# Kernel tuning notes

Measured on AMD Instinct MI355X. Metric: run time of the kernel, lower is better.

Reference implementation:

```python
import jax, jax.numpy as jnp
import numpy as np

H = 768       # hidden_size
NH = 12       # num_attention_heads
HD = H // NH  # head_size
FF = 3072     # intermediate_size
EPS = 1e-5


def _layernorm(x, g, b):
    m = jnp.mean(x, axis=-1, keepdims=True)
    v = jnp.var(x, axis=-1, keepdims=True)
    return (x - m) * jax.lax.rsqrt(v + EPS) * g + b


def setup_inputs() -> dict:
    key = jax.random.key(0)
    ks = jax.random.split(key, 12)
    B, Sq, Skv = 8, 1024, 1024
    s = 0.02
    return {
        "freq_hidden_states": jax.random.normal(ks[0], (B, Sq, H), jnp.float32),
        "image_hidden_states": jax.random.normal(ks[1], (B, Skv, H), jnp.float32),
        # attention projections (stored [in, out])
        "Wq": jax.random.normal(ks[2], (H, H), jnp.float32) * s,
        "bq": jnp.zeros((H,), jnp.float32),
        "Wk": jax.random.normal(ks[3], (H, H), jnp.float32) * s,
        "bk": jnp.zeros((H,), jnp.float32),
        "Wv": jax.random.normal(ks[4], (H, H), jnp.float32) * s,
        "bv": jnp.zeros((H,), jnp.float32),
        # layernorms
        "ln_att_g": jnp.ones((H,), jnp.float32),
        "ln_att_b": jnp.zeros((H,), jnp.float32),
        "ln_mlp_g": jnp.ones((H,), jnp.float32),
        "ln_mlp_b": jnp.zeros((H,), jnp.float32),
        # MLP
        "W1": jax.random.normal(ks[5], (H, FF), jnp.float32) * s,
        "b1": jnp.zeros((FF,), jnp.float32),
        "W2": jax.random.normal(ks[6], (FF, H), jnp.float32) * s,
        "b2": jnp.zeros((H,), jnp.float32),
    }


def reference(image_hidden_states, freq_hidden_states, Wq, bq, Wk, bk, Wv, bv,
              ln_att_g, ln_att_b, ln_mlp_g, ln_mlp_b, W1, b1, W2, b2):
    B, Sq, _ = freq_hidden_states.shape
    Skv = image_hidden_states.shape[1]
    # cross-attention: query from freq, key/value from image
    q = (freq_hidden_states @ Wq + bq).reshape(B, Sq, NH, HD)
    k = (image_hidden_states @ Wk + bk).reshape(B, Skv, NH, HD)
    v = (image_hidden_states @ Wv + bv).reshape(B, Skv, NH, HD)
    scores = jnp.einsum("bqhd,bkhd->bhqk", q, k) / jnp.sqrt(jnp.float32(HD))
    probs = jax.nn.softmax(scores, axis=-1)
    ctx = jnp.einsum("bhqk,bkhd->bqhd", probs, v).reshape(B, Sq, H)
    # residual with post-LN on the attention output
    h = freq_hidden_states + _layernorm(ctx, ln_att_g, ln_att_b)
    # MLP + residual with post-LN on the MLP output
    mlp = jax.nn.relu(h @ W1 + b1) @ W2 + b2
    return h + _layernorm(mlp, ln_mlp_g, ln_mlp_b)
```

## Files before the change

kernel.cpp:

```cpp
#include <hip/hip_runtime.h>
#include <hip/hip_bf16.h>

#define H 768
#define NH 12
#define HD 64
#define FF 3072
#define SQ 1024
#define SKV 1024

typedef __hip_bfloat16 bf16;
typedef __attribute__((ext_vector_type(8))) short short8;
typedef __attribute__((ext_vector_type(4))) float f32x4;

__device__ inline void gload16(const void* g, void* l) {
  __builtin_amdgcn_global_load_lds((const __attribute__((address_space(1))) void*)g,
                                   (__attribute__((address_space(3))) void*)l, 16, 0, 0);
}

__device__ inline float bf2f(unsigned short u) {
  unsigned int x = ((unsigned int)u) << 16;
  return __builtin_bit_cast(float, x);
}

__global__ __launch_bounds__(256) void cvt_bf16(const float* __restrict__ src,
                                                bf16* __restrict__ dst) {
  int i = blockIdx.x * 256 + threadIdx.x;
  float4 v = ((const float4*)src)[i];
  union { unsigned short u[4]; uint2 q; } o;
  bf16 t0 = __float2bfloat16(v.x); o.u[0] = *(unsigned short*)&t0;
  bf16 t1 = __float2bfloat16(v.y); o.u[1] = *(unsigned short*)&t1;
  bf16 t2 = __float2bfloat16(v.z); o.u[2] = *(unsigned short*)&t2;
  bf16 t3 = __float2bfloat16(v.w); o.u[3] = *(unsigned short*)&t3;
  ((uint2*)dst)[i] = o.q;
}

__global__ __launch_bounds__(256) void trans_cvt(const float* __restrict__ src,
                                                 bf16* __restrict__ dst, int Kd, int Nd) {
  __shared__ float tile[32][33];
  int n0 = blockIdx.x * 32, k0 = blockIdx.y * 32;
  int tx = threadIdx.x, ty = threadIdx.y;
#pragma unroll
  for (int i = 0; i < 4; ++i)
    tile[ty + i * 8][tx] = src[(size_t)(k0 + ty + i * 8) * Nd + n0 + tx];
  __syncthreads();
#pragma unroll
  for (int i = 0; i < 4; ++i)
    dst[(size_t)(n0 + ty + i * 8) * Kd + k0 + tx] = __float2bfloat16(tile[tx][ty + i * 8]);
}

template <int EPI>
__global__ __launch_bounds__(256) void gemm_bt(
    const bf16* __restrict__ A, const bf16* __restrict__ BT,
    const float* __restrict__ bias0, const float* __restrict__ bias1,
    void* __restrict__ out0, void* __restrict__ out1, int M, int N, int K) {
  __shared__ __align__(16) bf16 lA[128 * 64];
  __shared__ __align__(16) bf16 lB[128 * 64];
  const int t = threadIdx.x;
  const int lane = t & 63, w = t >> 6;
  const int wr = w >> 1, wc = w & 1;
  const int nt = N >> 7;
  const int nwg = gridDim.x;
  int bid = blockIdx.x;
  int logical = ((nwg & 7) == 0) ? ((bid & 7) * (nwg >> 3) + (bid >> 3)) : bid;
  const int m0 = (logical / nt) << 7;
  const int n0 = (logical % nt) << 7;

  const f32x4 fz = {0.f, 0.f, 0.f, 0.f};
  f32x4 acc[4][4];
#pragma unroll
  for (int i = 0; i < 4; ++i)
#pragma unroll
    for (int j = 0; j < 4; ++j) acc[i][j] = fz;

  for (int kt = 0; kt < K; kt += 64) {
#pragma unroll
    for (int i = 0; i < 4; ++i) {
      int idx = i * 256 + t;
      int row = idx >> 3;
      int chunk = (idx & 7) ^ (row & 7);
      gload16(A + (size_t)(m0 + row) * K + kt + chunk * 8, lA + (size_t)(i * 256 + w * 64) * 8);
    }
#pragma unroll
    for (int i = 0; i < 4; ++i) {
      int idx = i * 256 + t;
      int row = idx >> 3;
      int chunk = (idx & 7) ^ (row & 7);
      gload16(BT + (size_t)(n0 + row) * K + kt + chunk * 8, lB + (size_t)(i * 256 + w * 64) * 8);
    }
    __syncthreads();

    short8 af[2][4], bfv[2][4];
#pragma unroll
    for (int s = 0; s < 2; ++s) {
#pragma unroll
      for (int i = 0; i < 4; ++i) {
        int ra = wr * 64 + i * 16 + (lane & 15);
        int ca = (s * 4 + (lane >> 4)) ^ (ra & 7);
        af[s][i] = *(const short8*)&lA[ra * 64 + ca * 8];
        int rb = wc * 64 + i * 16 + (lane & 15);
        int cb = (s * 4 + (lane >> 4)) ^ (rb & 7);
        bfv[s][i] = *(const short8*)&lB[rb * 64 + cb * 8];
      }
    }
#pragma unroll
    for (int s = 0; s < 2; ++s)
#pragma unroll
      for (int i = 0; i < 4; ++i)
#pragma unroll
        for (int j = 0; j < 4; ++j)
          acc[i][j] = __builtin_amdgcn_mfma_f32_16x16x32_bf16(af[s][i], bfv[s][j], acc[i][j], 0, 0, 0);
    __syncthreads();
  }

#pragma unroll
  for (int i = 0; i < 4; ++i) {
    int mbase = m0 + wr * 64 + i * 16 + ((lane >> 4) << 2);
#pragma unroll
    for (int j = 0; j < 4; ++j) {
      int n = n0 + wc * 64 + j * 16 + (lane & 15);
#pragma unroll
      for (int r = 0; r < 4; ++r) {
        int m = mbase + r;
        float v = acc[i][j][r];
        if (EPI == 0) {
          v = (v + bias0[n]) * 0.180336880f;
          int hlin = (m >> 10) * NH + (n >> 6);
          ((bf16*)out0)[((size_t)hlin * SQ + (m & 1023)) * HD + (n & 63)] = __float2bfloat16(v);
        } else if (EPI == 1) {
          int sel = (n >= H);
          int nn = n - (sel ? H : 0);
          v += (sel ? bias1 : bias0)[nn];
          int hlin = (m >> 10) * NH + (nn >> 6);
          if (!sel)
            ((bf16*)out0)[((size_t)hlin * SKV + (m & 1023)) * HD + (nn & 63)] = __float2bfloat16(v);
          else
            ((bf16*)out1)[((size_t)hlin * HD + (nn & 63)) * SKV + (m & 1023)] = __float2bfloat16(v);
        } else if (EPI == 2) {
          v += bias0[n];
          v = fmaxf(v, 0.f);
          ((bf16*)out0)[(size_t)m * N + n] = __float2bfloat16(v);
        } else {
          v += bias0[n];
          ((bf16*)out0)[(size_t)m * N + n] = __float2bfloat16(v);
        }
      }
    }
  }
}

__global__ __launch_bounds__(512, 4) void attn_fwd(
    const bf16* __restrict__ Q,
    const bf16* __restrict__ Kg_,
    const bf16* __restrict__ VT,
    bf16* __restrict__ ctx, int nblk) {
  __shared__ __align__(16) bf16 Ks[2][64 * 64];
  __shared__ __align__(16) bf16 Vs[2][64 * 64];
  __shared__ __align__(16) bf16 PQ[8 * 16 * 72];

  const int t = threadIdx.x, lane = t & 63, w = t >> 6;
  int bid = blockIdx.x;
  int logical = ((nblk & 7) == 0) ? (bid & 7) * (nblk >> 3) + (bid >> 3) : bid;
  const int hl = logical >> 3;
  const int q0 = (logical & 7) << 7;
  const bf16* Qg = Q + ((size_t)hl * SQ + q0) * HD;
  const bf16* Kg = Kg_ + (size_t)hl * SKV * HD;
  const bf16* Vg = VT + (size_t)hl * HD * SKV;

#pragma unroll
  for (int rep = 0; rep < 2; ++rep) {
    int idx = rep * 512 + t;
    int row = idx >> 3;
    int chunk = (idx & 7) ^ (row & 7);
    gload16(Qg + (size_t)row * HD + chunk * 8, PQ + (size_t)(rep * 512 + w * 64) * 8);
  }
  {
    int row = t >> 3, chunk = (t & 7) ^ (row & 7);
    gload16(Kg + (size_t)row * HD + chunk * 8, &Ks[0][(size_t)w * 64 * 8]);
    gload16(Vg + (size_t)row * SKV + chunk * 8, &Vs[0][(size_t)w * 64 * 8]);
  }
  __syncthreads();

  short8 aq[2];
#pragma unroll
  for (int s = 0; s < 2; ++s) {
    int row = w * 16 + (lane & 15);
    int chunk = (s * 4 + (lane >> 4)) ^ (row & 7);
    aq[s] = *(const short8*)&PQ[row * 64 + chunk * 8];
  }
  __syncthreads();

  float l_r[4];
#pragma unroll
  for (int r = 0; r < 4; ++r) l_r[r] = 0.f;
  const f32x4 fz = {0.f, 0.f, 0.f, 0.f};
  f32x4 oacc[4];
#pragma unroll
  for (int j = 0; j < 4; ++j) oacc[j] = fz;

  bf16* Pw = PQ + w * (16 * 72);
  const short s1 = (short)0x3F80;
  const short8 ones = {s1, s1, s1, s1, s1, s1, s1, s1};

#pragma unroll 2
  for (int i = 0; i < 16; ++i) {
    const int buf = i & 1;
    if (i < 15) {
      int kvn = (i + 1) << 6;
      int row = t >> 3, chunk = (t & 7) ^ (row & 7);
      gload16(Kg + (size_t)(kvn + row) * HD + chunk * 8, &Ks[buf ^ 1][(size_t)w * 64 * 8]);
      gload16(Vg + (size_t)row * SKV + kvn + chunk * 8, &Vs[buf ^ 1][(size_t)w * 64 * 8]);
    }

    f32x4 sa[4];
#pragma unroll
    for (int n = 0; n < 4; ++n) sa[n] = fz;
    __builtin_amdgcn_s_setprio(1);
#pragma unroll
    for (int s = 0; s < 2; ++s)
#pragma unroll
      for (int n = 0; n < 4; ++n) {
        int rb = n * 16 + (lane & 15);
        int cb = (s * 4 + (lane >> 4)) ^ (rb & 7);
        short8 bk = *(const short8*)&Ks[buf][rb * 64 + cb * 8];
        sa[n] = __builtin_amdgcn_mfma_f32_16x16x32_bf16(aq[s], bk, sa[n], 0, 0, 0);
      }
    __builtin_amdgcn_s_setprio(0);

#pragma unroll
    for (int n = 0; n < 4; ++n)
#pragma unroll
      for (int r = 0; r < 4; ++r)
        Pw[(((lane >> 4) << 2) + r) * 72 + n * 16 + (lane & 15)] =
            __float2bfloat16(exp2f(sa[n][r]));

    f32x4 ld = fz;
    __builtin_amdgcn_s_setprio(1);
#pragma unroll
    for (int kk = 0; kk < 2; ++kk) {
      short8 pa = *(const short8*)&Pw[(lane & 15) * 72 + kk * 32 + ((lane >> 4) << 3)];
      ld = __builtin_amdgcn_mfma_f32_16x16x32_bf16(pa, ones, ld, 0, 0, 0);
#pragma unroll
      for (int j = 0; j < 4; ++j) {
        int rb = j * 16 + (lane & 15);
        int cb = (kk * 4 + (lane >> 4)) ^ (rb & 7);
        short8 bv = *(const short8*)&Vs[buf][rb * 64 + cb * 8];
        oacc[j] = __builtin_amdgcn_mfma_f32_16x16x32_bf16(pa, bv, oacc[j], 0, 0, 0);
      }
    }
    __builtin_amdgcn_s_setprio(0);
#pragma unroll
    for (int r = 0; r < 4; ++r) l_r[r] += ld[r];

    __syncthreads();
  }

  const int b = hl / NH, hh = hl % NH;
  float rl[4];
#pragma unroll
  for (int r = 0; r < 4; ++r) rl[r] = 1.0f / l_r[r];
#pragma unroll
  for (int j = 0; j < 4; ++j)
#pragma unroll
    for (int r = 0; r < 4; ++r) {
      int q = q0 + w * 16 + ((lane >> 4) << 2) + r;
      int d = j * 16 + (lane & 15);
      ctx[((size_t)b * SQ + q) * H + hh * HD + d] = __float2bfloat16(oacc[j][r] * rl[r]);
    }
}

__global__ __launch_bounds__(256) void ln_res(
    const bf16* __restrict__ x, const float* __restrict__ res,
    const float* __restrict__ g, const float* __restrict__ beta,
    float* __restrict__ o32, bf16* __restrict__ ob, int write_b) {
  const int row = blockIdx.x;
  const int t = threadIdx.x;
  float v[4];
  float s = 0.f, s2 = 0.f;
  if (t < 192) {
    ushort4 xv = ((const ushort4*)(x + (size_t)row * H))[t];
    v[0] = bf2f(xv.x); v[1] = bf2f(xv.y); v[2] = bf2f(xv.z); v[3] = bf2f(xv.w);
#pragma unroll
    for (int k = 0; k < 4; ++k) { s += v[k]; s2 += v[k] * v[k]; }
  } else {
#pragma unroll
    for (int k = 0; k < 4; ++k) v[k] = 0.f;
  }
#pragma unroll
  for (int off = 32; off > 0; off >>= 1) {
    s += __shfl_down(s, off);
    s2 += __shfl_down(s2, off);
  }
  __shared__ float red[8];
  if ((t & 63) == 0) { red[t >> 6] = s; red[4 + (t >> 6)] = s2; }
  __syncthreads();
  float st = red[0] + red[1] + red[2] + red[3];
  float s2t = red[4] + red[5] + red[6] + red[7];
  float mean = st * (1.f / 768.f);
  float var = s2t * (1.f / 768.f) - mean * mean;
  float rs = rsqrtf(var + 1e-5f);
  if (t < 192) {
    float4 rv = ((const float4*)(res + (size_t)row * H))[t];
    float4 gv = ((const float4*)g)[t];
    float4 bv = ((const float4*)beta)[t];
    float4 o;
    o.x = rv.x + (v[0] - mean) * rs * gv.x + bv.x;
    o.y = rv.y + (v[1] - mean) * rs * gv.y + bv.y;
    o.z = rv.z + (v[2] - mean) * rs * gv.z + bv.z;
    o.w = rv.w + (v[3] - mean) * rs * gv.w + bv.w;
    ((float4*)(o32 + (size_t)row * H))[t] = o;
    if (write_b) {
      union { unsigned short u[4]; uint2 q; } ob4;
      bf16 b0 = __float2bfloat16(o.x); ob4.u[0] = *(unsigned short*)&b0;
      bf16 b1 = __float2bfloat16(o.y); ob4.u[1] = *(unsigned short*)&b1;
      bf16 b2 = __float2bfloat16(o.z); ob4.u[2] = *(unsigned short*)&b2;
      bf16 b3 = __float2bfloat16(o.w); ob4.u[3] = *(unsigned short*)&b3;
      ((uint2*)(ob + (size_t)row * H))[t] = ob4.q;
    }
  }
}

extern "C" void kernel_launch(void* const* d_in, const int* in_sizes, int n_in,
                              void* d_out, int out_size, void* d_ws, size_t ws_size,
                              hipStream_t stream) {
  const float* freq  = (const float*)d_in[0];
  const float* image = (const float*)d_in[1];
  const float* Wq = (const float*)d_in[2];
  const float* bq = (const float*)d_in[3];
  const float* Wk = (const float*)d_in[4];
  const float* bk = (const float*)d_in[5];
  const float* Wv = (const float*)d_in[6];
  const float* bv = (const float*)d_in[7];
  const float* g1 = (const float*)d_in[8];
  const float* be1 = (const float*)d_in[9];
  const float* g2 = (const float*)d_in[10];
  const float* be2 = (const float*)d_in[11];
  const float* W1 = (const float*)d_in[12];
  const float* b1 = (const float*)d_in[13];
  const float* W2 = (const float*)d_in[14];
  const float* b2 = (const float*)d_in[15];

  const int Bc = in_sizes[0] / (SQ * H);
  const int M = Bc * SQ;

  char* p = (char*)d_ws;
  bf16* W1T = (bf16*)p;  p += (size_t)FF * H * 2;
  bf16* W2T = (bf16*)p;  p += (size_t)H * FF * 2;
  bf16* ctxb = (bf16*)p; p += (size_t)M * H * 2;
  float* h32 = (float*)p; p += (size_t)M * H * 4;
  bf16* hb = (bf16*)p;   p += (size_t)M * H * 2;
  char* U = p;
  bf16* freqb = (bf16*)U;
  bf16* imageb = (bf16*)(U + (size_t)M * H * 2);
  bf16* WTq   = (bf16*)(U + (size_t)2 * M * H * 2);
  bf16* WTkv  = (bf16*)(U + (size_t)2 * M * H * 2 + (size_t)H * H * 2);
  bf16* Qb    = (bf16*)(U + (size_t)2 * M * H * 2 + (size_t)3 * H * H * 2);
  bf16* Kbuf  = (bf16*)((char*)Qb + (size_t)M * H * 2);
  bf16* VTb   = (bf16*)((char*)Kbuf + (size_t)M * H * 2);
  bf16* mlp1  = (bf16*)U;
  bf16* mlp2b = ctxb;

  int nv4 = M * H / 4;
  cvt_bf16<<<nv4 / 256, 256, 0, stream>>>(freq, freqb);
  cvt_bf16<<<nv4 / 256, 256, 0, stream>>>(image, imageb);
  dim3 tb(32, 8);
  trans_cvt<<<dim3(H / 32, H / 32), tb, 0, stream>>>(Wq, WTq, H, H);
  trans_cvt<<<dim3(H / 32, H / 32), tb, 0, stream>>>(Wk, WTkv, H, H);
  trans_cvt<<<dim3(H / 32, H / 32), tb, 0, stream>>>(Wv, WTkv + (size_t)H * H, H, H);
  trans_cvt<<<dim3(FF / 32, H / 32), tb, 0, stream>>>(W1, W1T, H, FF);
  trans_cvt<<<dim3(H / 32, FF / 32), tb, 0, stream>>>(W2, W2T, FF, H);

  gemm_bt<0><<<(M / 128) * (H / 128), 256, 0, stream>>>(freqb, WTq, bq, nullptr, Qb, nullptr, M, H, H);
  gemm_bt<1><<<(M / 128) * (2 * H / 128), 256, 0, stream>>>(imageb, WTkv, bk, bv, Kbuf, VTb, M, 2 * H, H);
  int nblk = Bc * NH * (SQ / 128);
  attn_fwd<<<nblk, 512, 0, stream>>>(Qb, Kbuf, VTb, ctxb, nblk);
  ln_res<<<M, 256, 0, stream>>>(ctxb, freq, g1, be1, h32, hb, 1);
  gemm_bt<2><<<(M / 128) * (FF / 128), 256, 0, stream>>>(hb, W1T, b1, nullptr, mlp1, nullptr, M, FF, H);
  gemm_bt<3><<<(M / 128) * (H / 128), 256, 0, stream>>>(mlp1, W2T, b2, nullptr, mlp2b, nullptr, M, H, FF);
  ln_res<<<M, 256, 0, stream>>>(mlp2b, h32, g2, be2, (float*)d_out, nullptr, 0);
}
```

Before: 268.2 us.

## Fuse prep conversions into one launch and use narrower N tiles for H-wide GEMMs

Merges the two activation bf16 conversions and five weight transpose-converts into a single prep kernel that dispatches by block index, cutting seven launches down to one. Separately, the GEMM is templated on the N tile width, and the Q projection and W2 GEMMs (N=768) use 64-wide tiles. That doubles their workgroup count from 384 to 768 so more of the CUs are busy. The trade-off is less B-tile reuse per workgroup and a larger share of A loads in the narrow-tile GEMMs.

```diff
diff --git a/kernel.cpp b/kernel.cpp
--- a/kernel.cpp
+++ b/kernel.cpp
@@ -22,9 +22,8 @@
   return __builtin_bit_cast(float, x);
 }
 
-__global__ __launch_bounds__(256) void cvt_bf16(const float* __restrict__ src,
-                                                bf16* __restrict__ dst) {
-  int i = blockIdx.x * 256 + threadIdx.x;
+__device__ inline void cvt_body(const float* __restrict__ src, bf16* __restrict__ dst, int blk) {
+  int i = blk * 256 + threadIdx.x;
   float4 v = ((const float4*)src)[i];
   union { unsigned short u[4]; uint2 q; } o;
   bf16 t0 = __float2bfloat16(v.x); o.u[0] = *(unsigned short*)&t0;
@@ -34,43 +33,68 @@
   ((uint2*)dst)[i] = o.q;
 }
 
-__global__ __launch_bounds__(256) void trans_cvt(const float* __restrict__ src,
-                                                 bf16* __restrict__ dst, int Kd, int Nd) {
-  __shared__ float tile[32][33];
-  int n0 = blockIdx.x * 32, k0 = blockIdx.y * 32;
-  int tx = threadIdx.x, ty = threadIdx.y;
+__device__ inline void trans_body(const float* __restrict__ src, bf16* __restrict__ dst,
+                                  int Kd, int Nd, int blk, float* tile ) {
+  int ntx = Nd >> 5;
+  int n0 = (blk % ntx) << 5, k0 = (blk / ntx) << 5;
+  int tx = threadIdx.x & 31, ty = threadIdx.x >> 5;
 #pragma unroll
   for (int i = 0; i < 4; ++i)
-    tile[ty + i * 8][tx] = src[(size_t)(k0 + ty + i * 8) * Nd + n0 + tx];
+    tile[(ty + i * 8) * 33 + tx] = src[(size_t)(k0 + ty + i * 8) * Nd + n0 + tx];
   __syncthreads();
 #pragma unroll
   for (int i = 0; i < 4; ++i)
-    dst[(size_t)(n0 + ty + i * 8) * Kd + k0 + tx] = __float2bfloat16(tile[tx][ty + i * 8]);
-}
-
-template <int EPI>
+    dst[(size_t)(n0 + ty + i * 8) * Kd + k0 + tx] = __float2bfloat16(tile[tx * 33 + ty + i * 8]);
+}
+
+__global__ __launch_bounds__(256) void prep(
+    const float* freq, const float* image, bf16* freqb, bf16* imageb,
+    const float* Wq, const float* Wk, const float* Wv, const float* W1, const float* W2,
+    bf16* WTq, bf16* WTk, bf16* WTv, bf16* W1T, bf16* W2T, int c1) {
+  __shared__ float tile[32 * 33];
+  int b = blockIdx.x;
+  if (b < c1) { cvt_body(freq, freqb, b); return; }
+  b -= c1;
+  if (b < c1) { cvt_body(image, imageb, b); return; }
+  b -= c1;
+  const int TQ = (H / 32) * (H / 32);
+  const int T1 = (FF / 32) * (H / 32);
+  if (b < TQ)            { trans_body(Wq, WTq, H, H, b, tile); return; }
+  b -= TQ;
+  if (b < TQ)            { trans_body(Wk, WTk, H, H, b, tile); return; }
+  b -= TQ;
+  if (b < TQ)            { trans_body(Wv, WTv, H, H, b, tile); return; }
+  b -= TQ;
+  if (b < T1)            { trans_body(W1, W1T, H, FF, b, tile); return; }
+  b -= T1;
+  trans_body(W2, W2T, FF, H, b, tile);
+}
+
+template <int EPI, int BN>
 __global__ __launch_bounds__(256) void gemm_bt(
     const bf16* __restrict__ A, const bf16* __restrict__ BT,
     const float* __restrict__ bias0, const float* __restrict__ bias1,
     void* __restrict__ out0, void* __restrict__ out1, int M, int N, int K) {
+  constexpr int SI = BN / 32;
+  constexpr int JF = BN / 32;
   __shared__ __align__(16) bf16 lA[128 * 64];
-  __shared__ __align__(16) bf16 lB[128 * 64];
+  __shared__ __align__(16) bf16 lB[BN * 64];
   const int t = threadIdx.x;
   const int lane = t & 63, w = t >> 6;
   const int wr = w >> 1, wc = w & 1;
-  const int nt = N >> 7;
+  const int nt = N / BN;
   const int nwg = gridDim.x;
   int bid = blockIdx.x;
   int logical = ((nwg & 7) == 0) ? ((bid & 7) * (nwg >> 3) + (bid >> 3)) : bid;
   const int m0 = (logical / nt) << 7;
-  const int n0 = (logical % nt) << 7;
+  const int n0 = (logical % nt) * BN;
 
   const f32x4 fz = {0.f, 0.f, 0.f, 0.f};
-  f32x4 acc[4][4];
+  f32x4 acc[4][JF];
 #pragma unroll
   for (int i = 0; i < 4; ++i)
 #pragma unroll
-    for (int j = 0; j < 4; ++j) acc[i][j] = fz;
+    for (int j = 0; j < JF; ++j) acc[i][j] = fz;
 
   for (int kt = 0; kt < K; kt += 64) {
 #pragma unroll
@@ -81,7 +105,7 @@
       gload16(A + (size_t)(m0 + row) * K + kt + chunk * 8, lA + (size_t)(i * 256 + w * 64) * 8);
     }
 #pragma unroll
-    for (int i = 0; i < 4; ++i) {
+    for (int i = 0; i < SI; ++i) {
       int idx = i * 256 + t;
       int row = idx >> 3;
       int chunk = (idx & 7) ^ (row & 7);
@@ -89,7 +113,7 @@
     }
     __syncthreads();
 
-    short8 af[2][4], bfv[2][4];
+    short8 af[2][4], bfv[2][JF];
 #pragma unroll
     for (int s = 0; s < 2; ++s) {
 #pragma unroll
@@ -97,9 +121,12 @@
         int ra = wr * 64 + i * 16 + (lane & 15);
         int ca = (s * 4 + (lane >> 4)) ^ (ra & 7);
         af[s][i] = *(const short8*)&lA[ra * 64 + ca * 8];
-        int rb = wc * 64 + i * 16 + (lane & 15);
+      }
+#pragma unroll
+      for (int j = 0; j < JF; ++j) {
+        int rb = wc * (BN / 2) + j * 16 + (lane & 15);
         int cb = (s * 4 + (lane >> 4)) ^ (rb & 7);
-        bfv[s][i] = *(const short8*)&lB[rb * 64 + cb * 8];
+        bfv[s][j] = *(const short8*)&lB[rb * 64 + cb * 8];
       }
     }
 #pragma unroll
@@ -107,7 +134,7 @@
 #pragma unroll
       for (int i = 0; i < 4; ++i)
 #pragma unroll
-        for (int j = 0; j < 4; ++j)
+        for (int j = 0; j < JF; ++j)
           acc[i][j] = __builtin_amdgcn_mfma_f32_16x16x32_bf16(af[s][i], bfv[s][j], acc[i][j], 0, 0, 0);
     __syncthreads();
   }
@@ -116,8 +143,8 @@
   for (int i = 0; i < 4; ++i) {
     int mbase = m0 + wr * 64 + i * 16 + ((lane >> 4) << 2);
 #pragma unroll
-    for (int j = 0; j < 4; ++j) {
-      int n = n0 + wc * 64 + j * 16 + (lane & 15);
+    for (int j = 0; j < JF; ++j) {
+      int n = n0 + wc * (BN / 2) + j * 16 + (lane & 15);
 #pragma unroll
       for (int r = 0; r < 4; ++r) {
         int m = mbase + r;
@@ -359,22 +386,18 @@
   bf16* mlp1  = (bf16*)U;
   bf16* mlp2b = ctxb;
 
-  int nv4 = M * H / 4;
-  cvt_bf16<<<nv4 / 256, 256, 0, stream>>>(freq, freqb);
-  cvt_bf16<<<nv4 / 256, 256, 0, stream>>>(image, imageb);
-  dim3 tb(32, 8);
-  trans_cvt<<<dim3(H / 32, H / 32), tb, 0, stream>>>(Wq, WTq, H, H);
-  trans_cvt<<<dim3(H / 32, H / 32), tb, 0, stream>>>(Wk, WTkv, H, H);
-  trans_cvt<<<dim3(H / 32, H / 32), tb, 0, stream>>>(Wv, WTkv + (size_t)H * H, H, H);
-  trans_cvt<<<dim3(FF / 32, H / 32), tb, 0, stream>>>(W1, W1T, H, FF);
-  trans_cvt<<<dim3(H / 32, FF / 32), tb, 0, stream>>>(W2, W2T, FF, H);
-
-  gemm_bt<0><<<(M / 128) * (H / 128), 256, 0, stream>>>(freqb, WTq, bq, nullptr, Qb, nullptr, M, H, H);
-  gemm_bt<1><<<(M / 128) * (2 * H / 128), 256, 0, stream>>>(imageb, WTkv, bk, bv, Kbuf, VTb, M, 2 * H, H);
+  int c1 = M * H / 1024;
+  int nprep = 2 * c1 + 3 * ((H / 32) * (H / 32)) + (FF / 32) * (H / 32) + (H / 32) * (FF / 32);
+  prep<<<nprep, 256, 0, stream>>>(freq, image, freqb, imageb,
+                                  Wq, Wk, Wv, W1, W2,
+                                  WTq, WTkv, WTkv + (size_t)H * H, W1T, W2T, c1);
+
+  gemm_bt<0, 64><<<(M / 128) * (H / 64), 256, 0, stream>>>(freqb, WTq, bq, nullptr, Qb, nullptr, M, H, H);
+  gemm_bt<1, 128><<<(M / 128) * (2 * H / 128), 256, 0, stream>>>(imageb, WTkv, bk, bv, Kbuf, VTb, M, 2 * H, H);
   int nblk = Bc * NH * (SQ / 128);
   attn_fwd<<<nblk, 512, 0, stream>>>(Qb, Kbuf, VTb, ctxb, nblk);
   ln_res<<<M, 256, 0, stream>>>(ctxb, freq, g1, be1, h32, hb, 1);
-  gemm_bt<2><<<(M / 128) * (FF / 128), 256, 0, stream>>>(hb, W1T, b1, nullptr, mlp1, nullptr, M, FF, H);
-  gemm_bt<3><<<(M / 128) * (H / 128), 256, 0, stream>>>(mlp1, W2T, b2, nullptr, mlp2b, nullptr, M, H, FF);
+  gemm_bt<2, 128><<<(M / 128) * (FF / 128), 256, 0, stream>>>(hb, W1T, b1, nullptr, mlp1, nullptr, M, FF, H);
+  gemm_bt<3, 64><<<(M / 128) * (H / 64), 256, 0, stream>>>(mlp1, W2T, b2, nullptr, mlp2b, nullptr, M, H, FF);
   ln_res<<<M, 256, 0, stream>>>(mlp2b, h32, g2, be2, (float*)d_out, nullptr, 0);
 }
```

Result: faster. 246.8 us (-8.0%).
